# Kernel optimization log

Measured on AMD Instinct MI355X. Metric: run time of the kernel, lower is better.

The kernel has to match this reference:

```python
import jax, jax.numpy as jnp
import numpy as np

EPS = 1e-6


def setup_inputs() -> dict:
    key = jax.random.key(0)
    ks = jax.random.split(key, 7)
    T, B, D, n, r = 512, 32, 1024, 1024, 8
    x = jax.random.normal(ks[0], (T, B, D), dtype=jnp.float32)
    # xavier_uniform-like init for weights
    def xavier(k, shape):
        fan_in, fan_out = shape[1], shape[0]
        a = float(np.sqrt(6.0 / (fan_in + fan_out)))
        return jax.random.uniform(k, shape, dtype=jnp.float32, minval=-a, maxval=a)
    W_k = xavier(ks[1], (n, D))
    W_v = xavier(ks[2], (n, D))
    W_q = xavier(ks[3], (n, D))
    W_kr = xavier(ks[4], (r, n))
    U0 = jnp.zeros((B, n, r), dtype=jnp.float32)
    V0 = jax.random.normal(ks[5], (B, n, r), dtype=jnp.float32) * 0.01
    return {"x": x, "W_k": W_k, "W_v": W_v, "W_q": W_q, "W_kr": W_kr, "U0": U0, "V0": V0}


def reference(x, W_k, W_v, W_q, W_kr, U0, V0):
    # x: [T, B, D]; state S = U @ V^T with U,V: [B, n, r]
    k = jnp.einsum('tbd,nd->tbn', x, W_k)
    v = jnp.einsum('tbd,nd->tbn', x, W_v)
    q = jnp.einsum('tbd,nd->tbn', x, W_q)
    V = V0  # V is never updated in the recurrence

    def step(U, kvq):
        k_t, v_t, q_t = kvq  # each [B, n]
        k_norm = k_t / (jnp.linalg.norm(k_t, axis=-1, keepdims=True) + EPS)
        Vtk = jnp.einsum('bnr,bn->br', V, k_norm)
        retrieved = jnp.einsum('bnr,br->bn', U, Vtk)
        delta = v_t - retrieved
        k_r = k_norm @ W_kr.T  # [B, r]
        U_new = jnp.tanh(U + delta[:, :, None] * k_r[:, None, :])
        Vtq = jnp.einsum('bnr,bn->br', V, q_t)
        Sq = jnp.einsum('bnr,br->bn', U_new, Vtq)
        out = Sq * jax.nn.silu(Sq)
        return U_new, out

    U_final, output = jax.lax.scan(step, U0, (k, v, q))
    return output, (U_final, V)
```

## Files before the change

kernel.cpp:

```cpp
#include <hip/hip_runtime.h>
#include <hip/hip_bf16.h>

typedef __attribute__((ext_vector_type(8))) short short8;
typedef __attribute__((ext_vector_type(4))) short short4v;
typedef __attribute__((ext_vector_type(4))) float f32x4;
typedef unsigned short u16;

__device__ inline float b2f(u16 u) {
    unsigned int i = ((unsigned int)u) << 16;
    float f; __builtin_memcpy(&f, &i, 4); return f;
}
__device__ inline u16 f2b(float f) {
    unsigned int i; __builtin_memcpy(&i, &f, 4);
    unsigned int r = (i + 0x7FFFu + ((i >> 16) & 1u)) >> 16;
    return (u16)r;
}

__device__ inline float xsum32(float x) {
    unsigned u; __builtin_memcpy(&u, &x, 4);
    auto r = __builtin_amdgcn_permlane32_swap(u, u, false, false);
    unsigned s0 = r[0], s1 = r[1];
    float f0, f1; __builtin_memcpy(&f0, &s0, 4); __builtin_memcpy(&f1, &s1, 4);
    return f0 + f1;
}

#define GLDS(g, l) __builtin_amdgcn_global_load_lds( \
    (const __attribute__((address_space(1))) void*)(g), \
    (__attribute__((address_space(3))) void*)(l), 16, 0, 0)

#define KWAIT(N) asm volatile("s_waitcnt lgkmcnt(0)\n\t" \
                              "s_waitcnt vmcnt(" #N ")\n\t" \
                              "s_barrier" ::: "memory")

__global__ __launch_bounds__(256) void cvt_k(const float* __restrict__ src,
                                             u16* __restrict__ dst, int n4)
{
    const int i = blockIdx.x * blockDim.x + threadIdx.x;
    if (i < n4) {
        const f32x4 v = ((const f32x4*)src)[i];
        short4v o;
        o.x = (short)f2b(v.x); o.y = (short)f2b(v.y);
        o.z = (short)f2b(v.z); o.w = (short)f2b(v.w);
        ((short4v*)dst)[i] = o;
    }
}

__global__ __launch_bounds__(256) void vT_k(const float* __restrict__ V0,
                                            float* __restrict__ V0T)
{
    const int gid = blockIdx.x * 256 + threadIdx.x;
    const int b = gid >> 9, j = (gid >> 6) & 7, n0 = (gid & 63) * 16;
    const float* src = V0 + (long)b * 8192 + (long)n0 * 8 + j;
    float* dst = V0T + (long)b * 8192 + (long)j * 1024 + n0;
#pragma unroll
    for (int i = 0; i < 16; i += 4) {
        f32x4 o = { src[(i + 0) * 8], src[(i + 1) * 8],
                    src[(i + 2) * 8], src[(i + 3) * 8] };
        *(f32x4*)(dst + i) = o;
    }
}

__global__ __launch_bounds__(256) void foldq_k(const float* __restrict__ V0T,
                                               const float* __restrict__ Wq,
                                               float* __restrict__ Aq)
{
    const int rb = blockIdx.x >> 3, dc = blockIdx.x & 7;
    const int dl = threadIdx.x & 127, g = threadIdx.x >> 7;
    const int d = dc * 128 + dl;
    __shared__ float rs[8][1024];
    {
        float* rf = (float*)rs;
        const float* sp = V0T + (long)rb * 8192;
        for (int i = threadIdx.x; i < 8192; i += 256) rf[i] = sp[i];
    }
    __syncthreads();
    float acc[4] = {0.f, 0.f, 0.f, 0.f};
    const float* wp = Wq + d;
#pragma unroll 4
    for (int n = 0; n < 1024; ++n) {
        const float w = wp[(long)n * 1024];
        acc[0] = fmaf(rs[g * 4 + 0][n], w, acc[0]);
        acc[1] = fmaf(rs[g * 4 + 1][n], w, acc[1]);
        acc[2] = fmaf(rs[g * 4 + 2][n], w, acc[2]);
        acc[3] = fmaf(rs[g * 4 + 3][n], w, acc[3]);
    }
#pragma unroll
    for (int r = 0; r < 4; ++r)
        Aq[(long)(rb * 8 + g * 4 + r) * 1024 + d] = acc[r];
}

__global__ __launch_bounds__(512) void gemm256_kv(
    const u16* __restrict__ Xbf, const u16* __restrict__ Wbf,
    u16* __restrict__ Ko, u16* __restrict__ Vo)
{
    __shared__ u16 lds[65536];

    const int bid = blockIdx.x;
    const int swz = (bid & 7) * 64 + (bid >> 3);
    const int bm = swz >> 3, bnx = swz & 7;
    const int widx = bnx >> 2;
    const int nbase = (bnx & 3) * 256;
    const int m0 = bm * 256;
    const u16* Wp = Wbf + (long)widx * 1048576;
    u16* O = (widx == 0) ? Ko : Vo;

    const int tid = threadIdx.x;
    const int w = tid >> 6;
    const int lane = tid & 63;
    const int wm = (w >> 2) * 128;
    const int wn = (w & 3) * 64;
    const int ln = lane & 15, qd = lane >> 4;

    const int q8 = lane >> 3, s8 = lane & 7;
    const int cc = s8 ^ q8;
    const u16* p0; const u16* p1; const u16* p2; const u16* p3;
    {
        auto mk = [&](int l) -> const u16* {
            const int r = l * 64 + w * 8 + q8;
            return (cc < 4)
                ? (Xbf + (long)(m0 + r) * 1024 + cc * 8)
                : (Wp  + (long)(nbase + r) * 1024 + (cc - 4) * 8);
        };
        p0 = mk(0); p1 = mk(1); p2 = mk(2); p3 = mk(3);
    }

    int aoff[8], boff[4];
#pragma unroll
    for (int mf = 0; mf < 8; ++mf) {
        const int ro = wm + mf * 16 + ln;
        aoff[mf] = ro * 128 + ((qd ^ (ro & 7)) * 16);
    }
#pragma unroll
    for (int nf = 0; nf < 4; ++nf) {
        const int rb = wn + nf * 16 + ln;
        boff[nf] = rb * 128 + (((4 + qd) ^ (rb & 7)) * 16);
    }

    f32x4 acc[8][4];
#pragma unroll
    for (int i = 0; i < 8; ++i)
#pragma unroll
        for (int j = 0; j < 4; ++j) acc[i][j] = (f32x4){0.f, 0.f, 0.f, 0.f};

#pragma unroll
    for (int tt = 0; tt < 3; ++tt) {
        char* db = (char*)lds + tt * 32768 + w * 1024;
        GLDS(p0, db);
        GLDS(p1, db + 8192);
        GLDS(p2, db + 16384);
        GLDS(p3, db + 24576);
        p0 += 32; p1 += 32; p2 += 32; p3 += 32;
    }
    KWAIT(8);

    for (int t = 0; t < 32; ++t) {
        const char* bb = (const char*)lds + (t & 3) * 32768;
        short8 a[8], bfr[4];
#pragma unroll
        for (int mf = 0; mf < 4; ++mf) a[mf] = *(const short8*)(bb + aoff[mf]);
#pragma unroll
        for (int nf = 0; nf < 4; ++nf) bfr[nf] = *(const short8*)(bb + boff[nf]);
        if (t < 29) {
            char* db = (char*)lds + ((t + 3) & 3) * 32768 + w * 1024;
            GLDS(p0, db);
            GLDS(p1, db + 8192);
            p0 += 32; p1 += 32;
        }
        __builtin_amdgcn_s_setprio(1);
#pragma unroll
        for (int mf = 0; mf < 4; ++mf)
#pragma unroll
            for (int nf = 0; nf < 4; ++nf)
                acc[mf][nf] = __builtin_amdgcn_mfma_f32_16x16x32_bf16(
                    a[mf], bfr[nf], acc[mf][nf], 0, 0, 0);
        __builtin_amdgcn_s_setprio(0);
#pragma unroll
        for (int mf = 4; mf < 8; ++mf) a[mf] = *(const short8*)(bb + aoff[mf]);
        if (t < 29) {
            char* db = (char*)lds + ((t + 3) & 3) * 32768 + w * 1024;
            GLDS(p2, db + 16384);
            GLDS(p3, db + 24576);
            p2 += 32; p3 += 32;
        }
        __builtin_amdgcn_s_setprio(1);
#pragma unroll
        for (int mf = 4; mf < 8; ++mf)
#pragma unroll
            for (int nf = 0; nf < 4; ++nf)
                acc[mf][nf] = __builtin_amdgcn_mfma_f32_16x16x32_bf16(
                    a[mf], bfr[nf], acc[mf][nf], 0, 0, 0);
        __builtin_amdgcn_s_setprio(0);
        if (t < 29)       KWAIT(8);
        else if (t == 29) KWAIT(4);
        else if (t == 30) KWAIT(0);
    }

#pragma unroll
    for (int mf = 0; mf < 8; ++mf) {
#pragma unroll
        for (int nf = 0; nf < 4; ++nf) {
            const int r0 = m0 + wm + mf * 16 + qd * 4;
            const int c  = nbase + wn + nf * 16 + ln;
#pragma unroll
            for (int r = 0; r < 4; ++r)
                O[(long)(r0 + r) * 1024 + c] = f2b(acc[mf][nf][r]);
        }
    }
}

__global__ __launch_bounds__(256) void scal_k(
    const u16* __restrict__ K, const u16* __restrict__ X,
    const float* __restrict__ V0T, const float* __restrict__ Wkr,
    const float* __restrict__ Aq, float* __restrict__ S)
{
    const int b  = blockIdx.x & 31;
    const int t0 = (blockIdx.x >> 5) * 4;
    const int tid = threadIdx.x;
    const int j = tid & 7, c = tid >> 3;
    const int n0 = c * 32;

    f32x4 vv[8], ww[8], aqv[8];
    {
        const f32x4* vp = (const f32x4*)(V0T + (long)b * 8192 + (long)j * 1024 + n0);
        const f32x4* wp = (const f32x4*)(Wkr + (long)j * 1024 + n0);
        const f32x4* ap = (const f32x4*)(Aq + (long)(b * 8 + j) * 1024 + n0);
#pragma unroll
        for (int i = 0; i < 8; i++) { vv[i] = vp[i]; ww[i] = wp[i]; aqv[i] = ap[i]; }
    }

    float avk[4], akr[4], avq[4], ass[4];
#pragma unroll
    for (int dt = 0; dt < 4; dt++) { avk[dt] = akr[dt] = avq[dt] = ass[dt] = 0.f; }

#pragma unroll
    for (int dt = 0; dt < 4; dt++) {
        const long m = (long)(t0 + dt) * 32 + b;
        const short8* kp = (const short8*)(K + m * 1024 + n0);
        const short8* xp = (const short8*)(X + m * 1024 + n0);
#pragma unroll
        for (int i = 0; i < 4; i++) {
            const short8 kb = kp[i], xb = xp[i];
#pragma unroll
            for (int e = 0; e < 8; e++) {
                const int idx = i * 8 + e;
                const float kv = b2f((u16)kb[e]);
                const float xv = b2f((u16)xb[e]);
                const float vj = vv[idx >> 2][idx & 3];
                const float wj = ww[idx >> 2][idx & 3];
                const float aj = aqv[idx >> 2][idx & 3];
                avk[dt] = fmaf(vj, kv, avk[dt]);
                akr[dt] = fmaf(wj, kv, akr[dt]);
                avq[dt] = fmaf(aj, xv, avq[dt]);
                ass[dt] = fmaf(kv, kv, ass[dt]);
            }
        }
    }

    __shared__ float red[4][4][3][8];
    __shared__ float ssr[4][4];
    const int wave = tid >> 6, lane = tid & 63;
#pragma unroll
    for (int dt = 0; dt < 4; dt++) {
        float a = avk[dt], k2 = akr[dt], q = avq[dt], s = ass[dt];
#pragma unroll
        for (int off = 8; off < 64; off <<= 1) {
            a  += __shfl_xor(a,  off, 64);
            k2 += __shfl_xor(k2, off, 64);
            q  += __shfl_xor(q,  off, 64);
            s  += __shfl_xor(s,  off, 64);
        }
        if (lane < 8) {
            red[wave][dt][0][lane] = a;
            red[wave][dt][1][lane] = k2;
            red[wave][dt][2][lane] = q;
        }
        if (lane == 0) ssr[wave][dt] = s;
    }
    __syncthreads();
    if (tid < 128) {
        const int dt = tid >> 5, rr = tid & 31;
        if (rr < 24) {
            const int v = rr >> 3, jj = rr & 7;
            float s = red[0][dt][v][jj] + red[1][dt][v][jj] +
                      red[2][dt][v][jj] + red[3][dt][v][jj];
            if (v != 2) {
                const float n2 = ssr[0][dt] + ssr[1][dt] + ssr[2][dt] + ssr[3][dt];
                const float inv = 1.0f / (sqrtf(n2) + 1e-6f);
                s *= (v == 0) ? (0.5f * inv) : (2.0f * inv);
            } else {
                s *= 0.5f;
            }
            S[((long)b * 512 + t0 + dt) * 32 + v * 8 + jj] = s;
        }
    }
}

__global__ __launch_bounds__(128) void scan_k(
    const u16* __restrict__ Vbuf, const float* __restrict__ S,
    const float* __restrict__ U0, float* __restrict__ outp,
    float* __restrict__ Ufin)
{
    __shared__ float Sl[512 * 32];

    const int b = blockIdx.x >> 4;
    const int chunk = blockIdx.x & 15;
    const int wave = threadIdx.x >> 6, lane = threadIdx.x & 63;
    const int rh = lane >> 5;
    const int n = chunk * 64 + wave * 32 + (lane & 31);
    const int so = rh * 4;

    {
        const f32x4* Sg = (const f32x4*)(S + (long)b * 16384);
        f32x4* Sd = (f32x4*)Sl;
        for (int i = threadIdx.x; i < 4096; i += 128) Sd[i] = Sg[i];
    }

    float U[4];
    {
        const float* u0 = U0 + ((long)b * 1024 + n) * 8 + so;
#pragma unroll
        for (int j2 = 0; j2 < 4; j2++) U[j2] = 2.0f * u0[j2];
    }

    const u16* vp0 = Vbuf + (long)b * 1024 + n;
    u16 vnx[16];
#pragma unroll
    for (int i = 0; i < 16; i++) vnx[i] = vp0[(long)i * 32768];

    __syncthreads();

    f32x4 sb[4][3];
#pragma unroll
    for (int s = 0; s < 4; ++s)
#pragma unroll
        for (int r = 0; r < 3; ++r)
            sb[s][r] = *(const f32x4*)&Sl[s * 32 + r * 8 + so];

    float* op = outp + (long)b * 1024 + n;

    for (int t0 = 0; t0 < 512; t0 += 16) {
        float vcur[16];
#pragma unroll
        for (int i = 0; i < 16; i++) vcur[i] = b2f(vnx[i]);
        const int tn = (t0 + 16 < 512) ? (t0 + 16) : t0;
#pragma unroll
        for (int i = 0; i < 16; i++) vnx[i] = vp0[(long)(tn + i) * 32768];

#pragma unroll
        for (int i = 0; i < 16; i++) {
            const int t = t0 + i;
            const int slot = i & 3;
            const f32x4 a = sb[slot][0], Kk = sb[slot][1], Qq = sb[slot][2];

            float pr = fmaf(U[0], a.x, U[1] * a.y) + fmaf(U[2], a.z, U[3] * a.w);
            const float ret = xsum32(pr);
            const float delta = vcur[i] - ret;

            const float kr4[4] = {Kk.x, Kk.y, Kk.z, Kk.w};
            const float vq4[4] = {Qq.x, Qq.y, Qq.z, Qq.w};

            float sq0 = 0.f, sq1 = 0.f;
#pragma unroll
            for (int j2 = 0; j2 < 4; j2++) {
                const float xx = fmaf(delta, kr4[j2], U[j2]);
                const float e = __expf(xx);
                const float rc = __builtin_amdgcn_rcpf(e + 1.0f);
                const float u = fmaf(-4.0f, rc, 2.0f);
                U[j2] = u;
                if (j2 & 1) sq1 = fmaf(u, vq4[j2], sq1);
                else        sq0 = fmaf(u, vq4[j2], sq0);
            }

            const int tf = (t + 4 < 512) ? (t + 4) : 511;
#pragma unroll
            for (int r = 0; r < 3; r++)
                sb[slot][r] = *(const f32x4*)&Sl[tf * 32 + r * 8 + so];

            const float Sq = xsum32(sq0 + sq1);
            const float sg = __builtin_amdgcn_rcpf(1.0f + __expf(-Sq));
            const float o = Sq * Sq * sg;
            if (rh == 0) op[(long)t * 32768] = o;
        }
    }

    *(f32x4*)(Ufin + ((long)b * 1024 + n) * 8 + so) =
        (f32x4){0.5f * U[0], 0.5f * U[1], 0.5f * U[2], 0.5f * U[3]};
}

__global__ __launch_bounds__(256) void vcopy_k(const float* __restrict__ src,
                                               float* __restrict__ dst)
{
    const int i = blockIdx.x * blockDim.x + threadIdx.x;
    ((f32x4*)dst)[i] = ((const f32x4*)src)[i];
}

extern "C" void kernel_launch(void* const* d_in, const int* in_sizes, int n_in,
                              void* d_out, int out_size, void* d_ws, size_t ws_size,
                              hipStream_t stream)
{
    const float* x   = (const float*)d_in[0];
    const float* Wk  = (const float*)d_in[1];
    const float* Wv  = (const float*)d_in[2];
    const float* Wq  = (const float*)d_in[3];
    const float* Wkr = (const float*)d_in[4];
    const float* U0  = (const float*)d_in[5];
    const float* V0  = (const float*)d_in[6];
    float* out = (float*)d_out;

    char* ws = (char*)d_ws;
    u16*   Xbf = (u16*)(ws);
    u16*   Wbf = (u16*)(ws + 33554432);
    u16*   Kb  = (u16*)(ws + 39845888);
    u16*   Vb  = (u16*)(ws + 73400320);
    float* Aq  = (float*)(ws + 106954752);
    float* Sc  = (float*)(ws + 140509184);
    float* V0T = (float*)(ws + 142606336);

    cvt_k<<<16384, 256, 0, stream>>>(x,  Xbf,               4194304);
    cvt_k<<<1024,  256, 0, stream>>>(Wk, Wbf,                262144);
    cvt_k<<<1024,  256, 0, stream>>>(Wv, Wbf + 1048576,      262144);
    vT_k <<<64,    256, 0, stream>>>(V0, V0T);
    foldq_k<<<256, 256, 0, stream>>>(V0T, Wq, Aq);

    gemm256_kv<<<512, 512, 0, stream>>>(Xbf, Wbf, Kb, Vb);
    scal_k  <<<4096, 256, 0, stream>>>(Kb, Xbf, V0T, Wkr, Aq, Sc);
    scan_k  <<<512, 128, 0, stream>>>(Vb, Sc, U0, out, out + 16777216);
    vcopy_k <<<256, 256, 0, stream>>>(V0, out + 17039360);
}
```

Measured before the change: 506.8 us.

## Split foldq over n-chunks with vectorized register tiling and separate reduction

The V0^T·Wq fold kernel now splits the 1024-long n reduction into 8 chunks per batch. Each thread computes 4 output columns for all 8 ranks using float4 loads of Wq, in place of 1 column for 4 ranks. Partial sums go to a new workspace buffer and a new reduction kernel adds them. The aim is to cut the serial reduction length per block and the redundant Wq reads, at the cost of an extra launch and partial-sum traffic.

```diff
diff --git a/kernel.cpp b/kernel.cpp
--- a/kernel.cpp
+++ b/kernel.cpp
@@ -62,31 +62,65 @@
 
 __global__ __launch_bounds__(256) void foldq_k(const float* __restrict__ V0T,
                                                const float* __restrict__ Wq,
-                                               float* __restrict__ Aq)
-{
-    const int rb = blockIdx.x >> 3, dc = blockIdx.x & 7;
-    const int dl = threadIdx.x & 127, g = threadIdx.x >> 7;
-    const int d = dc * 128 + dl;
-    __shared__ float rs[8][1024];
+                                               float* __restrict__ Aqp)
+{
+    const int b  = blockIdx.x >> 3;
+    const int kc = blockIdx.x & 7;
+    const int tid = threadIdx.x;
+    const int d0 = tid * 4;
+
+    __shared__ float rs[8][128];
     {
-        float* rf = (float*)rs;
-        const float* sp = V0T + (long)rb * 8192;
-        for (int i = threadIdx.x; i < 8192; i += 256) rf[i] = sp[i];
+        const int j = tid >> 5, nn = (tid & 31) * 4;
+        *(f32x4*)&rs[j][nn] =
+            *(const f32x4*)(V0T + (long)b * 8192 + j * 1024 + kc * 128 + nn);
     }
     __syncthreads();
-    float acc[4] = {0.f, 0.f, 0.f, 0.f};
-    const float* wp = Wq + d;
+
+    f32x4 acc[8];
+#pragma unroll
+    for (int r = 0; r < 8; ++r) acc[r] = (f32x4){0.f, 0.f, 0.f, 0.f};
+
+    const float* wp = Wq + (long)(kc * 128) * 1024 + d0;
 #pragma unroll 4
-    for (int n = 0; n < 1024; ++n) {
-        const float w = wp[(long)n * 1024];
-        acc[0] = fmaf(rs[g * 4 + 0][n], w, acc[0]);
-        acc[1] = fmaf(rs[g * 4 + 1][n], w, acc[1]);
-        acc[2] = fmaf(rs[g * 4 + 2][n], w, acc[2]);
-        acc[3] = fmaf(rs[g * 4 + 3][n], w, acc[3]);
-    }
-#pragma unroll
-    for (int r = 0; r < 4; ++r)
-        Aq[(long)(rb * 8 + g * 4 + r) * 1024 + d] = acc[r];
+    for (int nb = 0; nb < 32; ++nb) {
+        const f32x4 w0 = *(const f32x4*)(wp);
+        const f32x4 w1 = *(const f32x4*)(wp + 1024);
+        const f32x4 w2 = *(const f32x4*)(wp + 2048);
+        const f32x4 w3 = *(const f32x4*)(wp + 3072);
+        wp += 4096;
+#pragma unroll
+        for (int r = 0; r < 8; ++r) {
+            const f32x4 rv = *(const f32x4*)&rs[r][nb * 4];
+            f32x4 a = acc[r];
+            a.x = fmaf(rv.x, w0.x, a.x); a.y = fmaf(rv.x, w0.y, a.y);
+            a.z = fmaf(rv.x, w0.z, a.z); a.w = fmaf(rv.x, w0.w, a.w);
+            a.x = fmaf(rv.y, w1.x, a.x); a.y = fmaf(rv.y, w1.y, a.y);
+            a.z = fmaf(rv.y, w1.z, a.z); a.w = fmaf(rv.y, w1.w, a.w);
+            a.x = fmaf(rv.z, w2.x, a.x); a.y = fmaf(rv.z, w2.y, a.y);
+            a.z = fmaf(rv.z, w2.z, a.z); a.w = fmaf(rv.z, w2.w, a.w);
+            a.x = fmaf(rv.w, w3.x, a.x); a.y = fmaf(rv.w, w3.y, a.y);
+            a.z = fmaf(rv.w, w3.z, a.z); a.w = fmaf(rv.w, w3.w, a.w);
+            acc[r] = a;
+        }
+    }
+
+#pragma unroll
+    for (int r = 0; r < 8; ++r)
+        *(f32x4*)(Aqp + (long)kc * 262144 + (long)(b * 8 + r) * 1024 + d0) = acc[r];
+}
+
+__global__ __launch_bounds__(256) void redq_k(const float* __restrict__ Aqp,
+                                              float* __restrict__ Aq)
+{
+    const int i = blockIdx.x * 256 + threadIdx.x;
+    f32x4 s = ((const f32x4*)Aqp)[i];
+#pragma unroll
+    for (int kc = 1; kc < 8; ++kc) {
+        const f32x4 p = ((const f32x4*)Aqp)[(long)kc * 65536 + i];
+        s.x += p.x; s.y += p.y; s.z += p.z; s.w += p.w;
+    }
+    ((f32x4*)Aq)[i] = s;
 }
 
 __global__ __launch_bounds__(512) void gemm256_kv(
@@ -413,6 +447,7 @@
     u16*   Kb  = (u16*)(ws + 39845888);
     u16*   Vb  = (u16*)(ws + 73400320);
     float* Aq  = (float*)(ws + 106954752);
+    float* Aqp = (float*)(ws + 108003328);
     float* Sc  = (float*)(ws + 140509184);
     float* V0T = (float*)(ws + 142606336);
 
@@ -420,7 +455,8 @@
     cvt_k<<<1024,  256, 0, stream>>>(Wk, Wbf,                262144);
     cvt_k<<<1024,  256, 0, stream>>>(Wv, Wbf + 1048576,      262144);
     vT_k <<<64,    256, 0, stream>>>(V0, V0T);
-    foldq_k<<<256, 256, 0, stream>>>(V0T, Wq, Aq);
+    foldq_k<<<256, 256, 0, stream>>>(V0T, Wq, Aqp);
+    redq_k <<<256, 256, 0, stream>>>(Aqp, Aq);
 
     gemm256_kv<<<512, 512, 0, stream>>>(Xbf, Wbf, Kb, Vb);
     scal_k  <<<4096, 256, 0, stream>>>(Kb, Xbf, V0T, Wkr, Aq, Sc);
```

Result: faster. 425.1 us (-16.1%).
